# Kernel optimization log

Hardware: AMD Instinct MI355X
Metric: run time of the kernel (lower is better)

Reference implementation:

```python
import jax, jax.numpy as jnp
import numpy as np

DEPTH = 6
NB_CLASSES = 10
INPUT_SIZE = 4096
N_INTERNAL = 2**DEPTH - 1  # 63
N_LEAVES = 2**DEPTH       # 64
T = 8192


def setup_inputs() -> dict:
    key = jax.random.key(0)
    k1, k2, k3, k4, k5 = jax.random.split(key, 5)
    input_traj = jax.random.normal(k1, (T, INPUT_SIZE), dtype=jnp.float32)
    # node gates: Linear(input_size, 1) per internal node, stacked [N, D]
    W = jax.random.normal(k2, (N_INTERNAL, INPUT_SIZE), dtype=jnp.float32) / np.sqrt(INPUT_SIZE)
    b = jax.random.normal(k3, (N_INTERNAL,), dtype=jnp.float32) * 0.01
    beta = jax.random.uniform(k4, (N_INTERNAL,), dtype=jnp.float32)  # torch.rand(1) per node
    leaf_dist = jax.random.uniform(k5, (N_LEAVES, NB_CLASSES), dtype=jnp.float32)
    class_reward = jnp.arange(NB_CLASSES, dtype=jnp.float32)
    return {"input_traj": input_traj, "W": W, "b": b, "beta": beta,
            "leaf_dist": leaf_dist, "class_reward": class_reward}


def reference(input_traj, W, b, beta, leaf_dist, class_reward):
    # Node gating probs for all T states and all internal nodes at once.
    # Original: sigmoid(beta * fc(x)) per node, per state. [T, N_INTERNAL]
    P = jax.nn.sigmoid(beta[None, :] * (input_traj @ W.T + b[None, :]))
    # Path probabilities down the complete binary tree (BFS/heap layout:
    # level k occupies node indices [2^k - 1, 2^(k+1) - 1)). child[0] gets p,
    # child[1] gets (1 - p).
    t = input_traj.shape[0]
    pp = jnp.ones((t, 1), dtype=P.dtype)
    offset = 0
    for k in range(DEPTH):
        n = 1 << k
        Pl = P[:, offset:offset + n]            # [T, n]
        pp = jnp.stack([pp * Pl, pp * (1.0 - Pl)], axis=-1).reshape(t, 2 * n)
        offset += n
    # pp: [T, N_LEAVES], leaves in left-to-right order.
    # Leaf reward: inner(class_reward, softmax(distribution)) per leaf. [L]
    leaf_r = jnp.sum(jax.nn.softmax(leaf_dist, axis=-1) * class_reward[None, :], axis=-1)
    # Trajectory reward: sum over states and leaves of path_prob * leaf reward.
    return jnp.sum(pp @ leaf_r)
```

## Files before the change

### kernel.cpp

```cpp
#include <hip/hip_runtime.h>
#include <hip/hip_bf16.h>

#define T_ROWS   8192
#define K_DIM    4096
#define N_INT    63
#define N_LEAF   64
#define NCLS     10

typedef __bf16 bf16x8 __attribute__((ext_vector_type(8)));
typedef __bf16 bf16x4 __attribute__((ext_vector_type(4)));
typedef float  f32x4  __attribute__((ext_vector_type(4)));

__global__ __launch_bounds__(256) void sdt_prep(
    const float* __restrict__ W,
    const float* __restrict__ leaf_dist,
    const float* __restrict__ class_reward,
    __bf16* __restrict__ Wb,
    float* __restrict__ leaf_r,
    float* __restrict__ out)
{
    int gid  = blockIdx.x * 256 + threadIdx.x;
    int base = gid * 4;
    int n    = base >> 12;
    bf16x4 v;
    if (n < N_INT) {
        const float4 w = *reinterpret_cast<const float4*>(W + base);
        v[0] = (__bf16)w.x; v[1] = (__bf16)w.y; v[2] = (__bf16)w.z; v[3] = (__bf16)w.w;
    } else {
        v[0] = (__bf16)0.0f; v[1] = (__bf16)0.0f; v[2] = (__bf16)0.0f; v[3] = (__bf16)0.0f;
    }
    *reinterpret_cast<bf16x4*>(Wb + base) = v;

    if (blockIdx.x == 0) {
        if (threadIdx.x < N_LEAF) {
            int i = threadIdx.x;
            float m = -1e30f;
            #pragma unroll
            for (int j = 0; j < NCLS; ++j) m = fmaxf(m, leaf_dist[i * NCLS + j]);
            float s = 0.0f, d = 0.0f;
            #pragma unroll
            for (int j = 0; j < NCLS; ++j) {
                float e = expf(leaf_dist[i * NCLS + j] - m);
                s += e;
                d += e * class_reward[j];
            }
            leaf_r[i] = d / s;
        } else if (threadIdx.x == N_LEAF) {
            out[0] = 0.0f;
        }
    }
}

__global__ __launch_bounds__(512, 4) void sdt_main(
    const float* __restrict__ X,
    const __bf16* __restrict__ Wb,
    const float* __restrict__ b,
    const float* __restrict__ beta,
    const float* __restrict__ leaf_r,
    float* __restrict__ out)
{
    __shared__ float red[8 * 16 * 65];
    __shared__ float Pbuf[16 * 64];
    __shared__ float sred[8];

    const int tid  = threadIdx.x;
    const int wid  = tid >> 6;
    const int lane = tid & 63;
    const int m16  = lane & 15;
    const int q    = lane >> 4;

    const int row0 = blockIdx.x * 16;
    const float* Arow = X + (size_t)(row0 + m16) * K_DIM;

    f32x4 acc[4];
    #pragma unroll
    for (int g = 0; g < 4; ++g) acc[g] = (f32x4){0.0f, 0.0f, 0.0f, 0.0f};

    const int kbase = wid * (K_DIM / 8);

    #pragma unroll 2
    for (int it = 0; it < 16; ++it) {
        const int k0 = kbase + it * 32 + q * 8;
        const f32x4 a0 = __builtin_nontemporal_load(
            reinterpret_cast<const f32x4*>(Arow + k0));
        const f32x4 a1 = __builtin_nontemporal_load(
            reinterpret_cast<const f32x4*>(Arow + k0 + 4));
        bf16x8 af;
        af[0] = (__bf16)a0[0]; af[1] = (__bf16)a0[1];
        af[2] = (__bf16)a0[2]; af[3] = (__bf16)a0[3];
        af[4] = (__bf16)a1[0]; af[5] = (__bf16)a1[1];
        af[6] = (__bf16)a1[2]; af[7] = (__bf16)a1[3];
        #pragma unroll
        for (int g = 0; g < 4; ++g) {
            const bf16x8 bf = *reinterpret_cast<const bf16x8*>(
                Wb + (size_t)(g * 16 + m16) * K_DIM + k0);
            acc[g] = __builtin_amdgcn_mfma_f32_16x16x32_bf16(af, bf, acc[g], 0, 0, 0);
        }
    }

    #pragma unroll
    for (int g = 0; g < 4; ++g)
        #pragma unroll
        for (int r = 0; r < 4; ++r)
            red[(wid * 16 + q * 4 + r) * 65 + g * 16 + m16] = acc[g][r];
    __syncthreads();

    for (int e = tid; e < 16 * 64; e += 512) {
        const int r = e >> 6, c = e & 63;
        float s = 0.0f;
        #pragma unroll
        for (int w = 0; w < 8; ++w) s += red[(w * 16 + r) * 65 + c];
        float P = 0.0f;
        if (c < N_INT) {
            const float z = beta[c] * (s + b[c]);
            P = 1.0f / (1.0f + __expf(-z));
        }
        Pbuf[r * 64 + c] = P;
    }
    __syncthreads();

    const int row  = tid >> 5;
    const int pair = tid & 31;
    float score = 0.0f;
    #pragma unroll
    for (int u = 0; u < 2; ++u) {
        const int leaf = pair * 2 + u;
        float prod = 1.0f;
        #pragma unroll
        for (int k = 0; k < 6; ++k) {
            const int node = ((1 << k) - 1) + (leaf >> (6 - k));
            const float p  = Pbuf[row * 64 + node];
            const int bit  = (leaf >> (5 - k)) & 1;
            prod *= bit ? (1.0f - p) : p;
        }
        score += prod * leaf_r[leaf];
    }

    #pragma unroll
    for (int off = 32; off > 0; off >>= 1)
        score += __shfl_down(score, off, 64);
    if (lane == 0) sred[wid] = score;
    __syncthreads();
    if (tid == 0) {
        float s = 0.0f;
        #pragma unroll
        for (int w = 0; w < 8; ++w) s += sred[w];
        atomicAdd(out, s);
    }
}

extern "C" void kernel_launch(void* const* d_in, const int* in_sizes, int n_in,
                              void* d_out, int out_size, void* d_ws, size_t ws_size,
                              hipStream_t stream)
{
    const float* X           = (const float*)d_in[0];
    const float* W           = (const float*)d_in[1];
    const float* b           = (const float*)d_in[2];
    const float* beta        = (const float*)d_in[3];
    const float* leaf_dist   = (const float*)d_in[4];
    const float* class_rew   = (const float*)d_in[5];
    float* out               = (float*)d_out;

    __bf16* Wb    = (__bf16*)d_ws;
    float*  leafr = (float*)((char*)d_ws + (size_t)N_LEAF * K_DIM * 2);

    sdt_prep<<<256, 256, 0, stream>>>(W, leaf_dist, class_rew, Wb, leafr, out);
    sdt_main<<<T_ROWS / 16, 512, 0, stream>>>(X, Wb, b, beta, leafr, out);
}
```

Baseline: 221.4 us.

## Halve block size and software-prefetch X tiles one iteration ahead

The main kernel goes from 512 to 256 threads per block, so each of the four waves covers twice as much K range, and the reduction and leaf-scoring stages are resized to match. The K loop now keeps a register double buffer, issuing the next X loads before converting and running MFMAs on the current tile, with the W row pointers precomputed. The aim is to hide global load latency for the memory-bound X stream. In exchange it raises register pressure and gives each block fewer waves to hide latency with.

New measurement: 226.7 us. 1.02x slower.

```diff
diff --git a/kernel.cpp b/kernel.cpp
--- a/kernel.cpp
+++ b/kernel.cpp
@@ -51,7 +51,7 @@
     }
 }
 
-__global__ __launch_bounds__(512, 4) void sdt_main(
+__global__ __launch_bounds__(256, 4) void sdt_main(
     const float* __restrict__ X,
     const __bf16* __restrict__ Wb,
     const float* __restrict__ b,
@@ -59,9 +59,9 @@
     const float* __restrict__ leaf_r,
     float* __restrict__ out)
 {
-    __shared__ float red[8 * 16 * 65];
+    __shared__ float red[4 * 16 * 65];
     __shared__ float Pbuf[16 * 64];
-    __shared__ float sred[8];
+    __shared__ float sred[4];
 
     const int tid  = threadIdx.x;
     const int wid  = tid >> 6;
@@ -70,32 +70,44 @@
     const int q    = lane >> 4;
 
     const int row0 = blockIdx.x * 16;
-    const float* Arow = X + (size_t)(row0 + m16) * K_DIM;
+    const int kbase = wid * (K_DIM / 4);
+
+    const f32x4* Ap = reinterpret_cast<const f32x4*>(
+        X + (size_t)(row0 + m16) * K_DIM + kbase + q * 8);
+    const __bf16* B0 = Wb + (size_t)(0 * 16 + m16) * K_DIM + kbase + q * 8;
+    const __bf16* B1 = Wb + (size_t)(1 * 16 + m16) * K_DIM + kbase + q * 8;
+    const __bf16* B2 = Wb + (size_t)(2 * 16 + m16) * K_DIM + kbase + q * 8;
+    const __bf16* B3 = Wb + (size_t)(3 * 16 + m16) * K_DIM + kbase + q * 8;
 
     f32x4 acc[4];
     #pragma unroll
     for (int g = 0; g < 4; ++g) acc[g] = (f32x4){0.0f, 0.0f, 0.0f, 0.0f};
 
-    const int kbase = wid * (K_DIM / 8);
+    f32x4 c0 = __builtin_nontemporal_load(Ap);
+    f32x4 c1 = __builtin_nontemporal_load(Ap + 1);
 
     #pragma unroll 2
-    for (int it = 0; it < 16; ++it) {
-        const int k0 = kbase + it * 32 + q * 8;
-        const f32x4 a0 = __builtin_nontemporal_load(
-            reinterpret_cast<const f32x4*>(Arow + k0));
-        const f32x4 a1 = __builtin_nontemporal_load(
-            reinterpret_cast<const f32x4*>(Arow + k0 + 4));
+    for (int it = 0; it < 32; ++it) {
+        f32x4 n0, n1;
+        if (it < 31) {
+            n0 = __builtin_nontemporal_load(Ap + (it + 1) * 8);
+            n1 = __builtin_nontemporal_load(Ap + (it + 1) * 8 + 1);
+        }
         bf16x8 af;
-        af[0] = (__bf16)a0[0]; af[1] = (__bf16)a0[1];
-        af[2] = (__bf16)a0[2]; af[3] = (__bf16)a0[3];
-        af[4] = (__bf16)a1[0]; af[5] = (__bf16)a1[1];
-        af[6] = (__bf16)a1[2]; af[7] = (__bf16)a1[3];
-        #pragma unroll
-        for (int g = 0; g < 4; ++g) {
-            const bf16x8 bf = *reinterpret_cast<const bf16x8*>(
-                Wb + (size_t)(g * 16 + m16) * K_DIM + k0);
-            acc[g] = __builtin_amdgcn_mfma_f32_16x16x32_bf16(af, bf, acc[g], 0, 0, 0);
-        }
+        af[0] = (__bf16)c0[0]; af[1] = (__bf16)c0[1];
+        af[2] = (__bf16)c0[2]; af[3] = (__bf16)c0[3];
+        af[4] = (__bf16)c1[0]; af[5] = (__bf16)c1[1];
+        af[6] = (__bf16)c1[2]; af[7] = (__bf16)c1[3];
+        const int ko = it * 32;
+        const bf16x8 bf0 = *reinterpret_cast<const bf16x8*>(B0 + ko);
+        const bf16x8 bf1 = *reinterpret_cast<const bf16x8*>(B1 + ko);
+        const bf16x8 bf2 = *reinterpret_cast<const bf16x8*>(B2 + ko);
+        const bf16x8 bf3 = *reinterpret_cast<const bf16x8*>(B3 + ko);
+        acc[0] = __builtin_amdgcn_mfma_f32_16x16x32_bf16(af, bf0, acc[0], 0, 0, 0);
+        acc[1] = __builtin_amdgcn_mfma_f32_16x16x32_bf16(af, bf1, acc[1], 0, 0, 0);
+        acc[2] = __builtin_amdgcn_mfma_f32_16x16x32_bf16(af, bf2, acc[2], 0, 0, 0);
+        acc[3] = __builtin_amdgcn_mfma_f32_16x16x32_bf16(af, bf3, acc[3], 0, 0, 0);
+        c0 = n0; c1 = n1;
     }
 
     #pragma unroll
@@ -105,11 +117,11 @@
             red[(wid * 16 + q * 4 + r) * 65 + g * 16 + m16] = acc[g][r];
     __syncthreads();
 
-    for (int e = tid; e < 16 * 64; e += 512) {
+    for (int e = tid; e < 16 * 64; e += 256) {
         const int r = e >> 6, c = e & 63;
         float s = 0.0f;
         #pragma unroll
-        for (int w = 0; w < 8; ++w) s += red[(w * 16 + r) * 65 + c];
+        for (int w = 0; w < 4; ++w) s += red[(w * 16 + r) * 65 + c];
         float P = 0.0f;
         if (c < N_INT) {
             const float z = beta[c] * (s + b[c]);
@@ -119,12 +131,12 @@
     }
     __syncthreads();
 
-    const int row  = tid >> 5;
-    const int pair = tid & 31;
+    const int row = tid >> 4;
+    const int t16 = tid & 15;
     float score = 0.0f;
     #pragma unroll
-    for (int u = 0; u < 2; ++u) {
-        const int leaf = pair * 2 + u;
+    for (int u = 0; u < 4; ++u) {
+        const int leaf = t16 * 4 + u;
         float prod = 1.0f;
         #pragma unroll
         for (int k = 0; k < 6; ++k) {
@@ -142,9 +154,7 @@
     if (lane == 0) sred[wid] = score;
     __syncthreads();
     if (tid == 0) {
-        float s = 0.0f;
-        #pragma unroll
-        for (int w = 0; w < 8; ++w) s += sred[w];
+        float s = sred[0] + sred[1] + sred[2] + sred[3];
         atomicAdd(out, s);
     }
 }
@@ -165,5 +175,5 @@
     float*  leafr = (float*)((char*)d_ws + (size_t)N_LEAF * K_DIM * 2);
 
     sdt_prep<<<256, 256, 0, stream>>>(W, leaf_dist, class_rew, Wb, leafr, out);
-    sdt_main<<<T_ROWS / 16, 512, 0, stream>>>(X, Wb, b, beta, leafr, out);
+    sdt_main<<<T_ROWS / 16, 256, 0, stream>>>(X, Wb, b, beta, leafr, out);
 }
```
